# Optimization experiments

Measured on AMD Instinct MI355X. Metric: run time of the kernel, lower is better.

## Reference

```python
import jax, jax.numpy as jnp
import numpy as np

EPS = 1e-6  # matches nn.CosineSimilarity(dim=1, eps=1e-6)

def setup_inputs() -> dict:
    key = jax.random.key(0)
    k_w, k_q = jax.random.split(key)
    V, D = 1000000, 128
    weight = jax.random.normal(k_w, (V, D), dtype=jnp.float32)
    query_idx = jax.random.randint(k_q, (1,), 0, V, dtype=jnp.int64)
    return {"weight": weight, "query_idx": query_idx, "top_n": 5}

def reference(weight, query_idx, top_n):
    # weight: [V, D] embedding table; query_idx: [1] int index
    q = weight[query_idx[0]]                       # [D]
    # cosine similarity of q vs every row, torch semantics:
    # sim = x.y / clamp(||x||*||y||, min=eps)
    dots = jnp.einsum('vd,d->v', weight, q)        # [V]
    q_norm = jnp.sqrt(jnp.sum(q * q))
    w_norms = jnp.sqrt(jnp.sum(weight * weight, axis=1))  # [V]
    sim = dots / jnp.maximum(q_norm * w_norms, EPS)
    vals, idx = jax.lax.top_k(sim, top_n)          # [top_n], [top_n]
    return vals, idx
```

## Files before the change

### kernel.cpp

```cpp
#include <hip/hip_runtime.h>
#include <math.h>

#define NB1 1024
#define TPB 256
#define HALVES_PER_BLOCK (TPB / 32)
#define NCAND (NB1 * 5)

constexpr float EPS = 1e-6f;

__device__ __forceinline__ bool better(float v, int i, float bv, int bi) {
    return (v > bv) || (v == bv && i < bi);
}

__global__ __launch_bounds__(TPB) void sim_block_topk(
    const float* __restrict__ W, const int* __restrict__ qidx,
    int V, float* __restrict__ bv, int* __restrict__ bi)
{
    const int tid  = threadIdx.x;
    const int l    = tid & 31;
    const int half = tid >> 5;
    const int halfGlobal = blockIdx.x * HALVES_PER_BLOCK + half;
    const int nHalves    = NB1 * HALVES_PER_BLOCK;

    const int q = qidx[0];
    const float4 qv = ((const float4*)(W + (size_t)q * 128))[l];

    float qn2 = qv.x*qv.x + qv.y*qv.y + qv.z*qv.z + qv.w*qv.w;
    #pragma unroll
    for (int m = 16; m >= 1; m >>= 1) qn2 += __shfl_xor(qn2, m);
    const float qn = sqrtf(qn2);

    float tv[5]; int ti[5];
    #pragma unroll
    for (int j = 0; j < 5; j++) { tv[j] = -INFINITY; ti[j] = 0x7fffffff; }

    for (int row = halfGlobal; row < V; row += nHalves) {
        const float4 wv = ((const float4*)(W + (size_t)row * 128))[l];
        float dot = wv.x*qv.x + wv.y*qv.y + wv.z*qv.z + wv.w*qv.w;
        float nr  = wv.x*wv.x + wv.y*wv.y + wv.z*wv.z + wv.w*wv.w;
        #pragma unroll
        for (int m = 16; m >= 1; m >>= 1) {
            dot += __shfl_xor(dot, m);
            nr  += __shfl_xor(nr,  m);
        }
        if (l == 0) {
            float sim = dot / fmaxf(qn * sqrtf(nr), EPS);
            if (sim > tv[4]) {
                float nv = sim; int ni = row;
                #pragma unroll
                for (int j = 0; j < 5; j++) {
                    bool b = better(nv, ni, tv[j], ti[j]);
                    float ov = tv[j]; int oi = ti[j];
                    if (b) { tv[j] = nv; ti[j] = ni; nv = ov; ni = oi; }
                }
            }
        }
    }

    __shared__ float s_v[HALVES_PER_BLOCK * 5];
    __shared__ int   s_i[HALVES_PER_BLOCK * 5];
    if (l == 0) {
        #pragma unroll
        for (int j = 0; j < 5; j++) { s_v[half*5 + j] = tv[j]; s_i[half*5 + j] = ti[j]; }
    }
    __syncthreads();
    if (tid == 0) {
        for (int k = 0; k < 5; k++) {
            float cv = -INFINITY; int ci = 0x7fffffff; int cp = 0;
            for (int e = 0; e < HALVES_PER_BLOCK * 5; e++) {
                if (better(s_v[e], s_i[e], cv, ci)) { cv = s_v[e]; ci = s_i[e]; cp = e; }
            }
            bv[blockIdx.x*5 + k] = cv;
            bi[blockIdx.x*5 + k] = ci;
            s_v[cp] = -INFINITY;
        }
    }
}

__global__ __launch_bounds__(256) void final_topk(
    const float* __restrict__ bv, const int* __restrict__ bi,
    float* __restrict__ out)
{
    __shared__ float s_v[NCAND];
    __shared__ int   s_i[NCAND];
    __shared__ float sw_v[4];
    __shared__ int   sw_i[4], sw_p[4];

    const int tid = threadIdx.x;
    for (int e = tid; e < NCAND; e += 256) { s_v[e] = bv[e]; s_i[e] = bi[e]; }
    __syncthreads();

    for (int k = 0; k < 5; k++) {
        float v = -INFINITY; int i = 0x7fffffff; int p = 0;
        for (int e = tid; e < NCAND; e += 256) {
            if (better(s_v[e], s_i[e], v, i)) { v = s_v[e]; i = s_i[e]; p = e; }
        }
        #pragma unroll
        for (int m = 32; m >= 1; m >>= 1) {
            float ov = __shfl_xor(v, m);
            int   oi = __shfl_xor(i, m);
            int   op = __shfl_xor(p, m);
            if (better(ov, oi, v, i)) { v = ov; i = oi; p = op; }
        }
        if ((tid & 63) == 0) { int w = tid >> 6; sw_v[w] = v; sw_i[w] = i; sw_p[w] = p; }
        __syncthreads();
        if (tid == 0) {
            for (int w = 1; w < 4; w++)
                if (better(sw_v[w], sw_i[w], sw_v[0], sw_i[0])) {
                    sw_v[0] = sw_v[w]; sw_i[0] = sw_i[w]; sw_p[0] = sw_p[w];
                }
            out[k]     = sw_v[0];
            out[5 + k] = (float)sw_i[0];
            s_v[sw_p[0]] = -INFINITY;
        }
        __syncthreads();
    }
}

extern "C" void kernel_launch(void* const* d_in, const int* in_sizes, int n_in,
                              void* d_out, int out_size, void* d_ws, size_t ws_size,
                              hipStream_t stream) {
    const float* W    = (const float*)d_in[0];
    const int*   qidx = (const int*)d_in[1];
    const int V = in_sizes[0] / 128;

    float* bv = (float*)d_ws;
    int*   bi = (int*)((char*)d_ws + (size_t)NB1 * 5 * sizeof(float));

    sim_block_topk<<<NB1, TPB, 0, stream>>>(W, qidx, V, bv, bi);
    final_topk<<<1, 256, 0, stream>>>(bv, bi, (float*)d_out);
}
```

Baseline: 667.6 us.

## Process each row with 4 lanes holding 8 float4s instead of 32-lane halves

Each row is now handled by a group of 4 lanes, and each lane loads 8 float4 chunks. The query is held in registers, so only two shuffle steps are needed per reduction instead of five, which cuts cross-lane shuffle overhead. Each wave now has 16 candidate leaders, so the per-block top-5 merge becomes a parallel wave-shuffle reduction over 320 candidates. The change adds register pressure, and per-lane memory access becomes strided chunks within a row.

```diff
diff --git a/kernel.cpp b/kernel.cpp
--- a/kernel.cpp
+++ b/kernel.cpp
@@ -3,7 +3,11 @@
 
 #define NB1 1024
 #define TPB 256
-#define HALVES_PER_BLOCK (TPB / 32)
+#define WAVES_PER_BLOCK (TPB / 64)
+#define GROUPS_PER_WAVE 16
+#define TOTAL_GROUPS (NB1 * WAVES_PER_BLOCK * GROUPS_PER_WAVE)
+#define NLEAD (TPB / 4)
+#define NBCAND (NLEAD * 5)
 #define NCAND (NB1 * 5)
 
 constexpr float EPS = 1e-6f;
@@ -17,33 +21,44 @@
     int V, float* __restrict__ bv, int* __restrict__ bi)
 {
     const int tid  = threadIdx.x;
-    const int l    = tid & 31;
-    const int half = tid >> 5;
-    const int halfGlobal = blockIdx.x * HALVES_PER_BLOCK + half;
-    const int nHalves    = NB1 * HALVES_PER_BLOCK;
+    const int lane = tid & 63;
+    const int sub  = lane & 3;
+    const int grp  = lane >> 2;
+    const int wave = tid >> 6;
+    const int groupGlobal =
+        (blockIdx.x * WAVES_PER_BLOCK + wave) * GROUPS_PER_WAVE + grp;
 
     const int q = qidx[0];
-    const float4 qv = ((const float4*)(W + (size_t)q * 128))[l];
 
-    float qn2 = qv.x*qv.x + qv.y*qv.y + qv.z*qv.z + qv.w*qv.w;
+    float4 qv[8];
+    const float4* Q4 = (const float4*)(W + (size_t)q * 128);
     #pragma unroll
-    for (int m = 16; m >= 1; m >>= 1) qn2 += __shfl_xor(qn2, m);
+    for (int j = 0; j < 8; j++) qv[j] = Q4[sub + 4 * j];
+
+    float qn2 = 0.f;
+    #pragma unroll
+    for (int j = 0; j < 8; j++)
+        qn2 += qv[j].x*qv[j].x + qv[j].y*qv[j].y + qv[j].z*qv[j].z + qv[j].w*qv[j].w;
+    qn2 += __shfl_xor(qn2, 1);
+    qn2 += __shfl_xor(qn2, 2);
     const float qn = sqrtf(qn2);
 
     float tv[5]; int ti[5];
     #pragma unroll
     for (int j = 0; j < 5; j++) { tv[j] = -INFINITY; ti[j] = 0x7fffffff; }
 
-    for (int row = halfGlobal; row < V; row += nHalves) {
-        const float4 wv = ((const float4*)(W + (size_t)row * 128))[l];
-        float dot = wv.x*qv.x + wv.y*qv.y + wv.z*qv.z + wv.w*qv.w;
-        float nr  = wv.x*wv.x + wv.y*wv.y + wv.z*wv.z + wv.w*wv.w;
+    for (int row = groupGlobal; row < V; row += TOTAL_GROUPS) {
+        const float4* Wr = (const float4*)(W + (size_t)row * 128);
+        float dot = 0.f, nr = 0.f;
         #pragma unroll
-        for (int m = 16; m >= 1; m >>= 1) {
-            dot += __shfl_xor(dot, m);
-            nr  += __shfl_xor(nr,  m);
+        for (int j = 0; j < 8; j++) {
+            float4 wv = Wr[sub + 4 * j];
+            dot += wv.x*qv[j].x + wv.y*qv[j].y + wv.z*qv[j].z + wv.w*qv[j].w;
+            nr  += wv.x*wv.x   + wv.y*wv.y   + wv.z*wv.z   + wv.w*wv.w;
         }
-        if (l == 0) {
+        dot += __shfl_xor(dot, 1); dot += __shfl_xor(dot, 2);
+        nr  += __shfl_xor(nr,  1); nr  += __shfl_xor(nr,  2);
+        if (sub == 0) {
             float sim = dot / fmaxf(qn * sqrtf(nr), EPS);
             if (sim > tv[4]) {
                 float nv = sim; int ni = row;
@@ -57,23 +72,42 @@
         }
     }
 
-    __shared__ float s_v[HALVES_PER_BLOCK * 5];
-    __shared__ int   s_i[HALVES_PER_BLOCK * 5];
-    if (l == 0) {
+    __shared__ float s_v[NBCAND];
+    __shared__ int   s_i[NBCAND];
+    __shared__ float sw_v[WAVES_PER_BLOCK];
+    __shared__ int   sw_i[WAVES_PER_BLOCK], sw_p[WAVES_PER_BLOCK];
+
+    if (sub == 0) {
+        const int leader = tid >> 2;
         #pragma unroll
-        for (int j = 0; j < 5; j++) { s_v[half*5 + j] = tv[j]; s_i[half*5 + j] = ti[j]; }
+        for (int j = 0; j < 5; j++) { s_v[leader*5 + j] = tv[j]; s_i[leader*5 + j] = ti[j]; }
     }
     __syncthreads();
-    if (tid == 0) {
-        for (int k = 0; k < 5; k++) {
-            float cv = -INFINITY; int ci = 0x7fffffff; int cp = 0;
-            for (int e = 0; e < HALVES_PER_BLOCK * 5; e++) {
-                if (better(s_v[e], s_i[e], cv, ci)) { cv = s_v[e]; ci = s_i[e]; cp = e; }
-            }
-            bv[blockIdx.x*5 + k] = cv;
-            bi[blockIdx.x*5 + k] = ci;
-            s_v[cp] = -INFINITY;
+
+    for (int k = 0; k < 5; k++) {
+        float v = -INFINITY; int i = 0x7fffffff; int p = 0;
+        for (int e = tid; e < NBCAND; e += TPB) {
+            if (better(s_v[e], s_i[e], v, i)) { v = s_v[e]; i = s_i[e]; p = e; }
         }
+        #pragma unroll
+        for (int m = 32; m >= 1; m >>= 1) {
+            float ov = __shfl_xor(v, m);
+            int   oi = __shfl_xor(i, m);
+            int   op = __shfl_xor(p, m);
+            if (better(ov, oi, v, i)) { v = ov; i = oi; p = op; }
+        }
+        if (lane == 0) { sw_v[wave] = v; sw_i[wave] = i; sw_p[wave] = p; }
+        __syncthreads();
+        if (tid == 0) {
+            for (int w = 1; w < WAVES_PER_BLOCK; w++)
+                if (better(sw_v[w], sw_i[w], sw_v[0], sw_i[0])) {
+                    sw_v[0] = sw_v[w]; sw_i[0] = sw_i[w]; sw_p[0] = sw_p[w];
+                }
+            bv[blockIdx.x*5 + k] = sw_v[0];
+            bi[blockIdx.x*5 + k] = sw_i[0];
+            s_v[sw_p[0]] = -INFINITY;
+        }
+        __syncthreads();
     }
 }
 
```

Result: no change. 661.9 us (-0.8%).
